# Optimization experiments

Hardware: AMD Instinct MI355X
Metric: run time of the kernel (lower is better)

Reference implementation:

```python
import jax, jax.numpy as jnp
import numpy as np

T, B, D, N = 256, 8, 256, 64  # target_length, batch, d_embed, multi_infer_num


def setup_inputs() -> dict:
    key = jax.random.key(0)
    k1, k2, k3 = jax.random.split(key, 3)
    positions = jax.random.randint(k1, (T, B), 0, N, dtype=jnp.int64)
    outputs = jax.random.normal(k2, (T, B, D), dtype=jnp.float32)
    table = jax.random.normal(k3, (N, D, D), dtype=jnp.float32)
    return {"positions": positions, "outputs": outputs, "table": table}


def reference(positions, outputs, table):
    # gather: [T,B] -> [T,B,D,D]
    pos_emb = table[positions]
    # per-position mat-vec: out[i,b,e] = sum_d pos_emb[i,b,d,e] * outputs[i,b,d]
    return jnp.einsum('ibde,ibd->ibe', pos_emb, outputs)
```

## Files before the change

kernel.cpp:

```cpp
#include <hip/hip_runtime.h>

#define D_ 256
#define N_ 64
#define JT 16
#define CS 4
#define CMAX 80
#define GRID (N_ * CS)

typedef __attribute__((ext_vector_type(8))) short short8;
typedef __attribute__((ext_vector_type(4))) float f32x4;

__global__ __launch_bounds__(512) void fused_mpt_mfma(
    const void* __restrict__ positions_raw, const float* __restrict__ outputs,
    const float* __restrict__ table, float* __restrict__ out) {
  __shared__ __align__(16) unsigned short vhi[16][264];
  __shared__ __align__(16) unsigned short vlo[16][264];
  __shared__ __align__(16) float red[4][64][4];
  __shared__ int sidx[CMAX];
  __shared__ int wcnt[8];

  const int b = blockIdx.x;
  const int linear = (b & 7) * (GRID / 8) + (b >> 3);
  const int n = linear >> 2;
  const int h = linear & 3;

  const int t = threadIdx.x;
  const int w = t >> 6;
  const int l = t & 63;
  const int kcol = w & 3;
  const int khalf = w >> 2;

  const int col = h * 64 + kcol * 16 + (l & 15);
  const int kg = (l >> 4) * 8;
  const int kbase = khalf * 128;
  const float* Mcol = table + (size_t)n * (D_ * D_) + col;

  const int* p32 = (const int*)positions_raw;
  const long long* p64 = (const long long*)positions_raw;

  const bool use64 = (__ballot(p32[2 * l + 1] != 0) == 0ull);

  int pv[4];
  const int idx0 = w * 256;
#pragma unroll
  for (int r = 0; r < 4; ++r) {
    const int idx = idx0 + r * 64 + l;
    pv[r] = use64 ? (int)p64[idx] : p32[idx];
  }
  __builtin_amdgcn_sched_barrier(0);

  float mb[4][8];
#pragma unroll
  for (int s = 0; s < 4; ++s) {
#pragma unroll
    for (int i = 0; i < 8; ++i)
      mb[s][i] = Mcol[(size_t)(kbase + s * 32 + kg + i) * D_];
  }
  __builtin_amdgcn_sched_barrier(0);

  unsigned long long msk[4];
  int cw = 0;
#pragma unroll
  for (int r = 0; r < 4; ++r) {
    msk[r] = __ballot(pv[r] == n);
    cw += __popcll(msk[r]);
  }
  if (l == 0) wcnt[w] = cw;
  __syncthreads();
  int c = 0, base = 0;
#pragma unroll
  for (int ww = 0; ww < 8; ++ww) {
    const int cc = wcnt[ww];
    if (ww < w) base += cc;
    c += cc;
  }
  if (c > CMAX) c = CMAX;
  if (c == 0) return;

  const unsigned long long lt = (1ull << l) - 1ull;
  int run = base;
#pragma unroll
  for (int r = 0; r < 4; ++r) {
    const int g = run + __popcll(msk[r] & lt);
    if (((msk[r] >> l) & 1ull) && g < CMAX) sidx[g] = idx0 + r * 64 + l;
    run += __popcll(msk[r]);
  }
  __syncthreads();

  const int dg = t & 255;
  const int half = t >> 8;
  float vr[8];
#pragma unroll
  for (int j = 0; j < 8; ++j) {
    const int q = half * 8 + j;
    const int idx = (q < c) ? sidx[q] : -1;
    vr[j] = (idx >= 0) ? outputs[(size_t)idx * D_ + dg] : 0.0f;
  }

  short8 BH[4], BL[4];
#pragma unroll
  for (int s = 0; s < 4; ++s) {
    union {
      short8 v;
      unsigned u[4];
    } H, L;
#pragma unroll
    for (int p = 0; p < 4; ++p) {
      const unsigned b0 = __float_as_uint(mb[s][2 * p]);
      const unsigned b1 = __float_as_uint(mb[s][2 * p + 1]);
      H.u[p] = (b0 >> 16) | (b1 & 0xffff0000u);
      const float l0 = mb[s][2 * p] - __uint_as_float(b0 & 0xffff0000u);
      const float l1 = mb[s][2 * p + 1] - __uint_as_float(b1 & 0xffff0000u);
      L.u[p] =
          (__float_as_uint(l0) >> 16) | (__float_as_uint(l1) & 0xffff0000u);
    }
    BH[s] = H.v;
    BL[s] = L.v;
  }

  const int arow = l & 15;
  const int G = (c + JT - 1) >> 4;

  for (int g = 0; g < G; ++g) {
#pragma unroll
    for (int j = 0; j < 8; ++j) {
      const int row = half * 8 + j;
      const float v = vr[j];
      const unsigned bv = __float_as_uint(v);
      vhi[row][dg] = (unsigned short)(bv >> 16);
      const float lf = v - __uint_as_float(bv & 0xffff0000u);
      vlo[row][dg] = (unsigned short)(__float_as_uint(lf) >> 16);
    }
    __syncthreads();

    if (g + 1 < G) {
#pragma unroll
      for (int j = 0; j < 8; ++j) {
        const int q = (g + 1) * JT + half * 8 + j;
        const int idx = (q < c) ? sidx[q] : -1;
        vr[j] = (idx >= 0) ? outputs[(size_t)idx * D_ + dg] : 0.0f;
      }
    }

    f32x4 accA = {0.f, 0.f, 0.f, 0.f};
    f32x4 accB = {0.f, 0.f, 0.f, 0.f};
#pragma unroll
    for (int s = 0; s < 4; ++s) {
      const short8 ahi = *(const short8*)&vhi[arow][kbase + s * 32 + kg];
      const short8 alo = *(const short8*)&vlo[arow][kbase + s * 32 + kg];
      accA = __builtin_amdgcn_mfma_f32_16x16x32_bf16(ahi, BH[s], accA, 0, 0, 0);
      accB = __builtin_amdgcn_mfma_f32_16x16x32_bf16(alo, BH[s], accB, 0, 0, 0);
      accA = __builtin_amdgcn_mfma_f32_16x16x32_bf16(ahi, BL[s], accA, 0, 0, 0);
    }
    const f32x4 acc = accA + accB;

    if (khalf == 0) {
      *(f32x4*)&red[kcol][l][0] = acc;
    }
    __syncthreads();
    if (khalf == 1) {
      const f32x4 p = *(const f32x4*)&red[kcol][l][0];
      const f32x4 ssum = acc + p;
#pragma unroll
      for (int r = 0; r < 4; ++r) {
        const int row = (l >> 4) * 4 + r;
        const int q = g * JT + row;
        if (q < c) {
          out[(size_t)sidx[q] * D_ + col] = ssum[r];
        }
      }
    }
    __syncthreads();
  }
}

extern "C" void kernel_launch(void* const* d_in, const int* in_sizes, int n_in,
                              void* d_out, int out_size, void* d_ws,
                              size_t ws_size, hipStream_t stream) {
  const void* positions = d_in[0];
  const float* outputs = (const float*)d_in[1];
  const float* table = (const float*)d_in[2];
  float* out = (float*)d_out;
  (void)d_ws;
  (void)ws_size;

  fused_mpt_mfma<<<GRID, 512, 0, stream>>>(positions, outputs, table, out);
}
```

Measured before the change: 13.23 us.

## Double-buffer LDS tiles, vectorize row loads, defer reduction to cut barriers

The staged activation tiles and the cross-wave reduction buffer are now double-buffered, so the reduction and store for group g-1 happen after the next barrier. This removes two of the three barriers per group iteration. Each thread now loads eight contiguous floats as two float4 and packs them into one bf16 hi/lo short8 store, instead of doing eight scalar loads and strided 16-bit stores. The int64 check is reworked to reuse the first int32 loads and reload as int64 only when all odd words are zero, which saves a dependent load before the table loads. The cost is double the LDS for these buffers and slightly more complex control flow.

Result: faster. 12.33 us (-6.8%).

```diff
diff --git a/kernel.cpp b/kernel.cpp
--- a/kernel.cpp
+++ b/kernel.cpp
@@ -13,9 +13,9 @@
 __global__ __launch_bounds__(512) void fused_mpt_mfma(
     const void* __restrict__ positions_raw, const float* __restrict__ outputs,
     const float* __restrict__ table, float* __restrict__ out) {
-  __shared__ __align__(16) unsigned short vhi[16][264];
-  __shared__ __align__(16) unsigned short vlo[16][264];
-  __shared__ __align__(16) float red[4][64][4];
+  __shared__ __align__(16) unsigned short vhi[2][16][272];
+  __shared__ __align__(16) unsigned short vlo[2][16][272];
+  __shared__ __align__(16) float red[2][4][64][4];
   __shared__ int sidx[CMAX];
   __shared__ int wcnt[8];
 
@@ -38,15 +38,10 @@
   const int* p32 = (const int*)positions_raw;
   const long long* p64 = (const long long*)positions_raw;
 
-  const bool use64 = (__ballot(p32[2 * l + 1] != 0) == 0ull);
-
   int pv[4];
   const int idx0 = w * 256;
 #pragma unroll
-  for (int r = 0; r < 4; ++r) {
-    const int idx = idx0 + r * 64 + l;
-    pv[r] = use64 ? (int)p64[idx] : p32[idx];
-  }
+  for (int r = 0; r < 4; ++r) pv[r] = p32[idx0 + r * 64 + l];
   __builtin_amdgcn_sched_barrier(0);
 
   float mb[4][8];
@@ -57,6 +52,15 @@
       mb[s][i] = Mcol[(size_t)(kbase + s * 32 + kg + i) * D_];
   }
   __builtin_amdgcn_sched_barrier(0);
+
+  unsigned long long nz_odd = 0ull;
+#pragma unroll
+  for (int r = 0; r < 4; ++r) nz_odd |= __ballot(pv[r] != 0);
+  const bool use64 = ((nz_odd & 0xAAAAAAAAAAAAAAAAull) == 0ull);
+  if (use64) {
+#pragma unroll
+    for (int r = 0; r < 4; ++r) pv[r] = (int)p64[idx0 + r * 64 + l];
+  }
 
   unsigned long long msk[4];
   int cw = 0;
@@ -87,14 +91,20 @@
   }
   __syncthreads();
 
-  const int dg = t & 255;
-  const int half = t >> 8;
-  float vr[8];
-#pragma unroll
-  for (int j = 0; j < 8; ++j) {
-    const int q = half * 8 + j;
-    const int idx = (q < c) ? sidx[q] : -1;
-    vr[j] = (idx >= 0) ? outputs[(size_t)idx * D_ + dg] : 0.0f;
+  const int srow = t & 15;
+  const int d0 = (t >> 4) * 8;
+
+  float4 va, vb;
+  {
+    const int idx = (srow < c) ? sidx[srow] : -1;
+    if (idx >= 0) {
+      const float* vp = &outputs[(size_t)idx * D_ + d0];
+      va = *(const float4*)vp;
+      vb = *(const float4*)(vp + 4);
+    } else {
+      va = make_float4(0.f, 0.f, 0.f, 0.f);
+      vb = make_float4(0.f, 0.f, 0.f, 0.f);
+    }
   }
 
   short8 BH[4], BL[4];
@@ -120,25 +130,53 @@
 
   const int arow = l & 15;
   const int G = (c + JT - 1) >> 4;
+  f32x4 accPrev = {0.f, 0.f, 0.f, 0.f};
 
   for (int g = 0; g < G; ++g) {
-#pragma unroll
-    for (int j = 0; j < 8; ++j) {
-      const int row = half * 8 + j;
-      const float v = vr[j];
-      const unsigned bv = __float_as_uint(v);
-      vhi[row][dg] = (unsigned short)(bv >> 16);
-      const float lf = v - __uint_as_float(bv & 0xffff0000u);
-      vlo[row][dg] = (unsigned short)(__float_as_uint(lf) >> 16);
-    }
+    const int cur = g & 1;
+
+    {
+      const float vv[8] = {va.x, va.y, va.z, va.w, vb.x, vb.y, vb.z, vb.w};
+      union {
+        short8 v;
+        unsigned u[4];
+      } H, L;
+#pragma unroll
+      for (int p = 0; p < 4; ++p) {
+        const unsigned b0 = __float_as_uint(vv[2 * p]);
+        const unsigned b1 = __float_as_uint(vv[2 * p + 1]);
+        H.u[p] = (b0 >> 16) | (b1 & 0xffff0000u);
+        const float l0 = vv[2 * p] - __uint_as_float(b0 & 0xffff0000u);
+        const float l1 = vv[2 * p + 1] - __uint_as_float(b1 & 0xffff0000u);
+        L.u[p] =
+            (__float_as_uint(l0) >> 16) | (__float_as_uint(l1) & 0xffff0000u);
+      }
+      *(short8*)&vhi[cur][srow][d0] = H.v;
+      *(short8*)&vlo[cur][srow][d0] = L.v;
+    }
+
+    if (g + 1 < G) {
+      const int q = (g + 1) * JT + srow;
+      const int idx = (q < c) ? sidx[q] : -1;
+      if (idx >= 0) {
+        const float* vp = &outputs[(size_t)idx * D_ + d0];
+        va = *(const float4*)vp;
+        vb = *(const float4*)(vp + 4);
+      } else {
+        va = make_float4(0.f, 0.f, 0.f, 0.f);
+        vb = make_float4(0.f, 0.f, 0.f, 0.f);
+      }
+    }
+
     __syncthreads();
 
-    if (g + 1 < G) {
-#pragma unroll
-      for (int j = 0; j < 8; ++j) {
-        const int q = (g + 1) * JT + half * 8 + j;
-        const int idx = (q < c) ? sidx[q] : -1;
-        vr[j] = (idx >= 0) ? outputs[(size_t)idx * D_ + dg] : 0.0f;
+    if (khalf == 1 && g > 0) {
+      const f32x4 p = *(const f32x4*)&red[1 - cur][kcol][l][0];
+      const f32x4 ssum = accPrev + p;
+#pragma unroll
+      for (int r = 0; r < 4; ++r) {
+        const int q = (g - 1) * JT + (l >> 4) * 4 + r;
+        if (q < c) out[(size_t)sidx[q] * D_ + col] = ssum[r];
       }
     }
 
@@ -146,8 +184,8 @@
     f32x4 accB = {0.f, 0.f, 0.f, 0.f};
 #pragma unroll
     for (int s = 0; s < 4; ++s) {
-      const short8 ahi = *(const short8*)&vhi[arow][kbase + s * 32 + kg];
-      const short8 alo = *(const short8*)&vlo[arow][kbase + s * 32 + kg];
+      const short8 ahi = *(const short8*)&vhi[cur][arow][kbase + s * 32 + kg];
+      const short8 alo = *(const short8*)&vlo[cur][arow][kbase + s * 32 + kg];
       accA = __builtin_amdgcn_mfma_f32_16x16x32_bf16(ahi, BH[s], accA, 0, 0, 0);
       accB = __builtin_amdgcn_mfma_f32_16x16x32_bf16(alo, BH[s], accB, 0, 0, 0);
       accA = __builtin_amdgcn_mfma_f32_16x16x32_bf16(ahi, BL[s], accA, 0, 0, 0);
@@ -155,22 +193,22 @@
     const f32x4 acc = accA + accB;
 
     if (khalf == 0) {
-      *(f32x4*)&red[kcol][l][0] = acc;
-    }
-    __syncthreads();
-    if (khalf == 1) {
-      const f32x4 p = *(const f32x4*)&red[kcol][l][0];
-      const f32x4 ssum = acc + p;
-#pragma unroll
-      for (int r = 0; r < 4; ++r) {
-        const int row = (l >> 4) * 4 + r;
-        const int q = g * JT + row;
-        if (q < c) {
-          out[(size_t)sidx[q] * D_ + col] = ssum[r];
-        }
-      }
-    }
-    __syncthreads();
+      *(f32x4*)&red[cur][kcol][l][0] = acc;
+    } else {
+      accPrev = acc;
+    }
+  }
+
+  __syncthreads();
+  if (khalf == 1) {
+    const int cur = (G - 1) & 1;
+    const f32x4 p = *(const f32x4*)&red[cur][kcol][l][0];
+    const f32x4 ssum = accPrev + p;
+#pragma unroll
+    for (int r = 0; r < 4; ++r) {
+      const int q = (G - 1) * JT + (l >> 4) * 4 + r;
+      if (q < c) out[(size_t)sidx[q] * D_ + col] = ssum[r];
+    }
   }
 }
 
```
